# Optimization experiments

Measured on AMD Instinct MI355X. Metric: run time of the kernel, lower is better.

## Reference

```python
import jax, jax.numpy as jnp
import numpy as np

B, S, D = 2, 2048, 1024
H = 16
HEAD_DIM = 64          # matches head_dim init arg; D // H == 64
HALF_WINDOW = 32       # local_window_size // 2
SCALE = HEAD_DIM ** -0.5


def setup_inputs() -> dict:
    key = jax.random.key(0)
    ks = jax.random.split(key, 6)
    std = 1.0 / np.sqrt(D)
    return {
        "x": jax.random.normal(ks[0], (B, S, D), dtype=jnp.float32),
        "Wq": jax.random.normal(ks[1], (D, D), dtype=jnp.float32) * std,
        "Wk": jax.random.normal(ks[2], (D, D), dtype=jnp.float32) * std,
        "Wv": jax.random.normal(ks[3], (D, D), dtype=jnp.float32) * std,
        "Wo": jax.random.normal(ks[4], (D, D), dtype=jnp.float32) * std,
        "bo": jnp.zeros((D,), dtype=jnp.float32),
    }


def reference(x, Wq, Wk, Wv, Wo, bo):
    b, s, d = x.shape
    h, hd = H, d // H

    def split_heads(y):  # [b, s, d] -> [b, h, s, hd]
        return y.reshape(b, s, h, hd).transpose(0, 2, 1, 3)

    q = split_heads(x @ Wq) * SCALE
    k = split_heads(x @ Wk)
    v = split_heads(x @ Wv)

    # dense scores [b, h, s, s] (module materializes full O(S^2) matrix)
    scores = jnp.einsum("bhqd,bhkd->bhqk", q, k)

    # local window |i-j| <= HALF_WINDOW combined with causal j <= i
    i = jnp.arange(s)
    local = jnp.abs(i[:, None] - i[None, :]) <= HALF_WINDOW
    causal = i[None, :] <= i[:, None]
    mask = local & causal  # [s, s]
    scores = jnp.where(mask[None, None, :, :], scores, -jnp.inf)

    attn = jax.nn.softmax(scores, axis=-1)  # diagonal always valid -> no NaN
    out = jnp.einsum("bhqk,bhkd->bhqd", attn, v)
    out = out.transpose(0, 2, 1, 3).reshape(b, s, d)  # merge heads
    return out @ Wo + bo
```

## Files before the change

kernel.cpp:

```cpp
#include <hip/hip_runtime.h>
#include <hip/hip_bf16.h>

typedef __bf16 bf16_t;
typedef __bf16 bf16x8 __attribute__((ext_vector_type(8)));
typedef __bf16 bf16x4 __attribute__((ext_vector_type(4)));
typedef float  f32x4  __attribute__((ext_vector_type(4)));

#define B_   2
#define S_   2048
#define D_   1024
#define H_   16
#define HD_  64
#define HW   32
#define SCALE_ 0.125f

__device__ __forceinline__ void gl_lds16(const bf16_t* g, bf16_t* l) {
  __builtin_amdgcn_global_load_lds(
      (const __attribute__((address_space(1))) void*)g,
      (__attribute__((address_space(3))) void*)l, 16, 0, 0);
}

__global__ __launch_bounds__(256) void k_convert_x(const float* __restrict__ X,
                                                   bf16_t* __restrict__ Xb) {
  int i = blockIdx.x * 256 + threadIdx.x;
  const float4 a = ((const float4*)X)[i * 2];
  const float4 b = ((const float4*)X)[i * 2 + 1];
  bf16x8 r;
  r[0] = (bf16_t)a.x; r[1] = (bf16_t)a.y; r[2] = (bf16_t)a.z; r[3] = (bf16_t)a.w;
  r[4] = (bf16_t)b.x; r[5] = (bf16_t)b.y; r[6] = (bf16_t)b.z; r[7] = (bf16_t)b.w;
  ((bf16x8*)Xb)[i] = r;
}

__global__ __launch_bounds__(256) void k_convw(const float* __restrict__ W0,
                                               const float* __restrict__ W1,
                                               const float* __restrict__ W2,
                                               const float* __restrict__ W3,
                                               bf16_t* __restrict__ Wt) {
  __shared__ bf16_t t[64][72];
  int bid = blockIdx.x;
  int wsel = bid >> 8;
  const float* W = (wsel == 0) ? W0 : (wsel == 1) ? W1 : (wsel == 2) ? W2 : W3;
  bf16_t* dst = Wt + (size_t)wsel * D_ * D_;
  int tile = bid & 255;
  int k0 = (tile >> 4) * 64, n0 = (tile & 15) * 64;
  int tid = threadIdx.x;
  int r = tid >> 4, c4 = (tid & 15) * 4;
#pragma unroll
  for (int i = 0; i < 4; ++i) {
    int row = i * 16 + r;
    float4 v = *(const float4*)(W + (size_t)(k0 + row) * D_ + n0 + c4);
    t[row][c4 + 0] = (bf16_t)v.x;
    t[row][c4 + 1] = (bf16_t)v.y;
    t[row][c4 + 2] = (bf16_t)v.z;
    t[row][c4 + 3] = (bf16_t)v.w;
  }
  __syncthreads();
#pragma unroll
  for (int i = 0; i < 4; ++i) {
    int row = i * 16 + r;
    bf16x4 o;
    o[0] = t[c4 + 0][row];
    o[1] = t[c4 + 1][row];
    o[2] = t[c4 + 2][row];
    o[3] = t[c4 + 3][row];
    *(bf16x4*)(dst + (size_t)(n0 + row) * D_ + k0 + c4) = o;
  }
}

__global__ __launch_bounds__(256) void k_gemm_qkv(const bf16_t* __restrict__ X,
                                                  const bf16_t* __restrict__ Wt,
                                                  bf16_t* __restrict__ Q,
                                                  bf16_t* __restrict__ K,
                                                  bf16_t* __restrict__ V) {
  __shared__ bf16_t sA[128 * 32];
  __shared__ bf16_t sB[128 * 32];
  int bid = blockIdx.x;
  int mt = bid & 31, nt = bid >> 5;
  int wsel = nt >> 3;
  int n0 = (nt & 7) * 128, m0 = mt * 128;
  const bf16_t* Wp = Wt + (size_t)wsel * D_ * D_;
  int tid = threadIdx.x, lane = tid & 63, wave = tid >> 6;
  int wr = (wave >> 1) * 64, wc = (wave & 1) * 64;
  int r0 = wave * 32 + (lane >> 2);
  int ce = (lane & 3) * 8;
  const bf16_t* gA0 = X + (size_t)(m0 + r0) * D_ + ce;
  const bf16_t* gB0 = Wp + (size_t)(n0 + r0) * D_ + ce;
  bf16_t* lA0 = sA + wave * 1024;
  bf16_t* lB0 = sB + wave * 1024;
  f32x4 acc[4][4] = {};
  int kq = (lane >> 4) * 8, rl = lane & 15;
  for (int kt = 0; kt < D_; kt += 32) {
    __syncthreads();
    gl_lds16(gA0 + kt, lA0);
    gl_lds16(gA0 + kt + (size_t)16 * D_, lA0 + 512);
    gl_lds16(gB0 + kt, lB0);
    gl_lds16(gB0 + kt + (size_t)16 * D_, lB0 + 512);
    __syncthreads();
    bf16x8 af[4], bfr[4];
#pragma unroll
    for (int m = 0; m < 4; ++m)
      af[m] = *(const bf16x8*)&sA[(wr + m * 16 + rl) * 32 + kq];
#pragma unroll
    for (int n = 0; n < 4; ++n)
      bfr[n] = *(const bf16x8*)&sB[(wc + n * 16 + rl) * 32 + kq];
#pragma unroll
    for (int m = 0; m < 4; ++m)
#pragma unroll
      for (int n = 0; n < 4; ++n)
        acc[m][n] = __builtin_amdgcn_mfma_f32_16x16x32_bf16(af[m], bfr[n], acc[m][n], 0, 0, 0);
  }
  float qscale = (wsel == 0) ? SCALE_ : 1.0f;
#pragma unroll
  for (int m = 0; m < 4; ++m) {
#pragma unroll
    for (int n = 0; n < 4; ++n) {
#pragma unroll
      for (int r = 0; r < 4; ++r) {
        int gm = m0 + wr + m * 16 + (lane >> 4) * 4 + r;
        int gn = n0 + wc + n * 16 + rl;
        int b = gm >> 11, s = gm & 2047;
        int h = gn >> 6, hd = gn & 63;
        bf16_t val = (bf16_t)(acc[m][n][r] * qscale);
        if (wsel == 0)
          Q[(((size_t)(b * H_ + h)) * S_ + s) * HD_ + hd] = val;
        else if (wsel == 1)
          K[(((size_t)(b * H_ + h)) * S_ + s) * HD_ + hd] = val;
        else
          V[(((size_t)(b * H_ + h)) * HD_ + hd) * S_ + s] = val;
      }
    }
  }
}

__global__ __launch_bounds__(256) void k_gemm_out(const bf16_t* __restrict__ A,
                                                  const bf16_t* __restrict__ Wp,
                                                  const float* __restrict__ bo,
                                                  float* __restrict__ out) {
  __shared__ bf16_t sA[128 * 32];
  __shared__ bf16_t sB[128 * 32];
  int bid = blockIdx.x;
  int mt = bid & 31, nt = bid >> 5;
  int n0 = nt * 128, m0 = mt * 128;
  int tid = threadIdx.x, lane = tid & 63, wave = tid >> 6;
  int wr = (wave >> 1) * 64, wc = (wave & 1) * 64;
  int r0 = wave * 32 + (lane >> 2);
  int ce = (lane & 3) * 8;
  const bf16_t* gA0 = A + (size_t)(m0 + r0) * D_ + ce;
  const bf16_t* gB0 = Wp + (size_t)(n0 + r0) * D_ + ce;
  bf16_t* lA0 = sA + wave * 1024;
  bf16_t* lB0 = sB + wave * 1024;
  f32x4 acc[4][4] = {};
  int kq = (lane >> 4) * 8, rl = lane & 15;
  for (int kt = 0; kt < D_; kt += 32) {
    __syncthreads();
    gl_lds16(gA0 + kt, lA0);
    gl_lds16(gA0 + kt + (size_t)16 * D_, lA0 + 512);
    gl_lds16(gB0 + kt, lB0);
    gl_lds16(gB0 + kt + (size_t)16 * D_, lB0 + 512);
    __syncthreads();
    bf16x8 af[4], bfr[4];
#pragma unroll
    for (int m = 0; m < 4; ++m)
      af[m] = *(const bf16x8*)&sA[(wr + m * 16 + rl) * 32 + kq];
#pragma unroll
    for (int n = 0; n < 4; ++n)
      bfr[n] = *(const bf16x8*)&sB[(wc + n * 16 + rl) * 32 + kq];
#pragma unroll
    for (int m = 0; m < 4; ++m)
#pragma unroll
      for (int n = 0; n < 4; ++n)
        acc[m][n] = __builtin_amdgcn_mfma_f32_16x16x32_bf16(af[m], bfr[n], acc[m][n], 0, 0, 0);
  }
#pragma unroll
  for (int m = 0; m < 4; ++m) {
#pragma unroll
    for (int n = 0; n < 4; ++n) {
#pragma unroll
      for (int r = 0; r < 4; ++r) {
        int gm = m0 + wr + m * 16 + (lane >> 4) * 4 + r;
        int gn = n0 + wc + n * 16 + rl;
        out[(size_t)gm * D_ + gn] = acc[m][n][r] + bo[gn];
      }
    }
  }
}

#define QB 64
#define KW 112
#define KLP 72
#define VTP 120

__global__ __launch_bounds__(256) void k_attn(const bf16_t* __restrict__ Q,
                                              const bf16_t* __restrict__ K,
                                              const bf16_t* __restrict__ Vt,
                                              bf16_t* __restrict__ O) {
  __shared__ bf16_t sK[KW][KLP];
  __shared__ bf16_t sV[HD_][VTP];
  __shared__ bf16_t sQ[QB][KLP];
  __shared__ bf16_t sP[4][16][KLP];
  int bid = blockIdx.x;
  int qb = bid & 31, bh = bid >> 5;
  int q0 = qb * QB;
  const bf16_t* Kp = K + (size_t)bh * S_ * HD_;
  const bf16_t* Vp = Vt + (size_t)bh * HD_ * S_;
  const bf16_t* Qp = Q + (size_t)bh * S_ * HD_;
  int tid = threadIdx.x;
  int wk0b = q0 - HW;
  for (int idx = tid; idx < KW * 8; idx += 256) {
    int row = idx >> 3, c8 = (idx & 7) * 8;
    int kg = wk0b + row;
    kg = kg < 0 ? 0 : (kg > S_ - 1 ? S_ - 1 : kg);
    *(bf16x8*)&sK[row][c8] = *(const bf16x8*)(Kp + (size_t)kg * HD_ + c8);
  }
  for (int idx = tid; idx < HD_ * 14; idx += 256) {
    int row = idx / 14, c8 = (idx % 14) * 8;
    int ks = wk0b + c8;
    ks = ks < 0 ? 0 : (ks > S_ - 8 ? S_ - 8 : ks);
    *(bf16x8*)&sV[row][c8] = *(const bf16x8*)(Vp + (size_t)row * S_ + ks);
  }
  for (int idx = tid; idx < QB * 8; idx += 256) {
    int row = idx >> 3, c8 = (idx & 7) * 8;
    *(bf16x8*)&sQ[row][c8] = *(const bf16x8*)(Qp + (size_t)(q0 + row) * HD_ + c8);
  }
  __syncthreads();
  int lane = tid & 63, wave = tid >> 6;
  int rl = lane & 15, hi = lane >> 4;
  int wko = wave * 16;
  f32x4 accs[4] = {};
#pragma unroll
  for (int ds = 0; ds < 2; ++ds) {
    bf16x8 qf = *(const bf16x8*)&sQ[wave * 16 + rl][ds * 32 + hi * 8];
#pragma unroll
    for (int kb = 0; kb < 4; ++kb) {
      bf16x8 kf = *(const bf16x8*)&sK[wko + kb * 16 + rl][ds * 32 + hi * 8];
      accs[kb] = __builtin_amdgcn_mfma_f32_16x16x32_bf16(kf, qf, accs[kb], 0, 0, 0);
    }
  }
  float p[4][4];
  float mx = -1e30f;
#pragma unroll
  for (int kb = 0; kb < 4; ++kb) {
#pragma unroll
    for (int r = 0; r < 4; ++r) {
      int kl = kb * 16 + hi * 4 + r;
      bool valid = (kl >= rl) && (kl <= rl + HW) && (wk0b + wko + kl >= 0);
      float s = valid ? accs[kb][r] : -1e30f;
      p[kb][r] = s;
      mx = fmaxf(mx, s);
    }
  }
  mx = fmaxf(mx, __shfl_xor(mx, 16));
  mx = fmaxf(mx, __shfl_xor(mx, 32));
  float sum = 0.f;
#pragma unroll
  for (int kb = 0; kb < 4; ++kb)
#pragma unroll
    for (int r = 0; r < 4; ++r) {
      p[kb][r] = __expf(p[kb][r] - mx);
      sum += p[kb][r];
    }
  sum += __shfl_xor(sum, 16);
  sum += __shfl_xor(sum, 32);
  float inv = 1.f / sum;
#pragma unroll
  for (int kb = 0; kb < 4; ++kb) {
    bf16x4 pv;
#pragma unroll
    for (int r = 0; r < 4; ++r) pv[r] = (bf16_t)(p[kb][r] * inv);
    *(bf16x4*)&sP[wave][rl][kb * 16 + hi * 4] = pv;
  }
  f32x4 acco[4] = {};
#pragma unroll
  for (int ks = 0; ks < 2; ++ks) {
    bf16x8 aP = *(const bf16x8*)&sP[wave][rl][ks * 32 + hi * 8];
#pragma unroll
    for (int n = 0; n < 4; ++n) {
      bf16x8 bV = *(const bf16x8*)&sV[n * 16 + rl][wko + ks * 32 + hi * 8];
      acco[n] = __builtin_amdgcn_mfma_f32_16x16x32_bf16(aP, bV, acco[n], 0, 0, 0);
    }
  }
  int b = bh >> 4, h = bh & 15;
#pragma unroll
  for (int n = 0; n < 4; ++n) {
#pragma unroll
    for (int r = 0; r < 4; ++r) {
      int qgl = q0 + wave * 16 + hi * 4 + r;
      int d = n * 16 + rl;
      O[((size_t)(b * S_ + qgl)) * D_ + h * HD_ + d] = (bf16_t)acco[n][r];
    }
  }
}

extern "C" void kernel_launch(void* const* d_in, const int* in_sizes, int n_in,
                              void* d_out, int out_size, void* d_ws, size_t ws_size,
                              hipStream_t stream) {
  const float* x  = (const float*)d_in[0];
  const float* Wq = (const float*)d_in[1];
  const float* Wk = (const float*)d_in[2];
  const float* Wv = (const float*)d_in[3];
  const float* Wo = (const float*)d_in[4];
  const float* bo = (const float*)d_in[5];
  float* out = (float*)d_out;
  char* ws = (char*)d_ws;
  bf16_t* xb = (bf16_t*)(ws);
  bf16_t* wt = (bf16_t*)(ws + (size_t)(8 << 20));
  bf16_t* qb = (bf16_t*)(ws + (size_t)(16 << 20));
  bf16_t* kb = (bf16_t*)(ws + (size_t)(24 << 20));
  bf16_t* vb = (bf16_t*)(ws + (size_t)(32 << 20));
  bf16_t* ob = (bf16_t*)(ws + (size_t)(40 << 20));

  hipLaunchKernelGGL(k_convert_x, dim3(2048), dim3(256), 0, stream, x, xb);
  hipLaunchKernelGGL(k_convw, dim3(1024), dim3(256), 0, stream, Wq, Wk, Wv, Wo, wt);
  hipLaunchKernelGGL(k_gemm_qkv, dim3(768), dim3(256), 0, stream, xb, wt, qb, kb, vb);
  hipLaunchKernelGGL(k_attn, dim3(1024), dim3(256), 0, stream, qb, kb, vb, ob);
  hipLaunchKernelGGL(k_gemm_out, dim3(256), dim3(256), 0, stream,
                     ob, wt + (size_t)3 * D_ * D_, bo, out);
}
```

Measured before the change: 88.24 us.

## Double-buffer GEMM LDS loads, vectorize QKV stores via LDS, merge conversion kernels

Both GEMM kernels now double-buffer their LDS tiles, so the next K-slice loads while MFMAs run on the current one, and each iteration needs one barrier instead of two. The QKV epilogue stages results through an LDS bounce buffer so Q/K and the transposed V are written as 16-byte vector stores rather than scattered 2-byte stores. The x and weight conversion kernels are merged into one launch. The cost is double the LDS per block, which may reduce occupancy, plus extra barriers in the epilogue.

```diff
diff --git a/kernel.cpp b/kernel.cpp
--- a/kernel.cpp
+++ b/kernel.cpp
@@ -13,6 +13,8 @@
 #define HD_  64
 #define HW   32
 #define SCALE_ 0.125f
+#define NT_  32
+#define BPAD 136
 
 __device__ __forceinline__ void gl_lds16(const bf16_t* g, bf16_t* l) {
   __builtin_amdgcn_global_load_lds(
@@ -20,30 +22,32 @@
       (__attribute__((address_space(3))) void*)l, 16, 0, 0);
 }
 
-__global__ __launch_bounds__(256) void k_convert_x(const float* __restrict__ X,
-                                                   bf16_t* __restrict__ Xb) {
-  int i = blockIdx.x * 256 + threadIdx.x;
-  const float4 a = ((const float4*)X)[i * 2];
-  const float4 b = ((const float4*)X)[i * 2 + 1];
-  bf16x8 r;
-  r[0] = (bf16_t)a.x; r[1] = (bf16_t)a.y; r[2] = (bf16_t)a.z; r[3] = (bf16_t)a.w;
-  r[4] = (bf16_t)b.x; r[5] = (bf16_t)b.y; r[6] = (bf16_t)b.z; r[7] = (bf16_t)b.w;
-  ((bf16x8*)Xb)[i] = r;
-}
-
-__global__ __launch_bounds__(256) void k_convw(const float* __restrict__ W0,
-                                               const float* __restrict__ W1,
-                                               const float* __restrict__ W2,
-                                               const float* __restrict__ W3,
-                                               bf16_t* __restrict__ Wt) {
+__global__ __launch_bounds__(256) void k_conv(const float* __restrict__ X,
+                                              const float* __restrict__ W0,
+                                              const float* __restrict__ W1,
+                                              const float* __restrict__ W2,
+                                              const float* __restrict__ W3,
+                                              bf16_t* __restrict__ Xb,
+                                              bf16_t* __restrict__ Wt) {
   __shared__ bf16_t t[64][72];
   int bid = blockIdx.x;
-  int wsel = bid >> 8;
+  int tid = threadIdx.x;
+  if (bid < 2048) {
+    int i = bid * 256 + tid;
+    const float4 a = ((const float4*)X)[i * 2];
+    const float4 b = ((const float4*)X)[i * 2 + 1];
+    bf16x8 r;
+    r[0] = (bf16_t)a.x; r[1] = (bf16_t)a.y; r[2] = (bf16_t)a.z; r[3] = (bf16_t)a.w;
+    r[4] = (bf16_t)b.x; r[5] = (bf16_t)b.y; r[6] = (bf16_t)b.z; r[7] = (bf16_t)b.w;
+    ((bf16x8*)Xb)[i] = r;
+    return;
+  }
+  int wb = bid - 2048;
+  int wsel = wb >> 8;
   const float* W = (wsel == 0) ? W0 : (wsel == 1) ? W1 : (wsel == 2) ? W2 : W3;
   bf16_t* dst = Wt + (size_t)wsel * D_ * D_;
-  int tile = bid & 255;
+  int tile = wb & 255;
   int k0 = (tile >> 4) * 64, n0 = (tile & 15) * 64;
-  int tid = threadIdx.x;
   int r = tid >> 4, c4 = (tid & 15) * 4;
 #pragma unroll
   for (int i = 0; i < 4; ++i) {
@@ -72,8 +76,7 @@
                                                   bf16_t* __restrict__ Q,
                                                   bf16_t* __restrict__ K,
                                                   bf16_t* __restrict__ V) {
-  __shared__ bf16_t sA[128 * 32];
-  __shared__ bf16_t sB[128 * 32];
+  __shared__ bf16_t smem[4][128 * 32];
   int bid = blockIdx.x;
   int mt = bid & 31, nt = bid >> 5;
   int wsel = nt >> 3;
@@ -85,48 +88,89 @@
   int ce = (lane & 3) * 8;
   const bf16_t* gA0 = X + (size_t)(m0 + r0) * D_ + ce;
   const bf16_t* gB0 = Wp + (size_t)(n0 + r0) * D_ + ce;
-  bf16_t* lA0 = sA + wave * 1024;
-  bf16_t* lB0 = sB + wave * 1024;
+  int lofs = wave * 1024;
   f32x4 acc[4][4] = {};
-  int kq = (lane >> 4) * 8, rl = lane & 15;
-  for (int kt = 0; kt < D_; kt += 32) {
-    __syncthreads();
-    gl_lds16(gA0 + kt, lA0);
-    gl_lds16(gA0 + kt + (size_t)16 * D_, lA0 + 512);
-    gl_lds16(gB0 + kt, lB0);
-    gl_lds16(gB0 + kt + (size_t)16 * D_, lB0 + 512);
-    __syncthreads();
+  int kq = (lane >> 4) * 8, rl = lane & 15, hi = lane >> 4;
+  gl_lds16(gA0, &smem[0][lofs]);
+  gl_lds16(gA0 + (size_t)16 * D_, &smem[0][lofs + 512]);
+  gl_lds16(gB0, &smem[2][lofs]);
+  gl_lds16(gB0 + (size_t)16 * D_, &smem[2][lofs + 512]);
+  __syncthreads();
+  int cur = 0;
+  for (int t = 0; t < NT_; ++t) {
+    if (t + 1 < NT_) {
+      int kt = (t + 1) * 32, nb = cur ^ 1;
+      gl_lds16(gA0 + kt, &smem[nb][lofs]);
+      gl_lds16(gA0 + kt + (size_t)16 * D_, &smem[nb][lofs + 512]);
+      gl_lds16(gB0 + kt, &smem[2 + nb][lofs]);
+      gl_lds16(gB0 + kt + (size_t)16 * D_, &smem[2 + nb][lofs + 512]);
+    }
     bf16x8 af[4], bfr[4];
 #pragma unroll
     for (int m = 0; m < 4; ++m)
-      af[m] = *(const bf16x8*)&sA[(wr + m * 16 + rl) * 32 + kq];
+      af[m] = *(const bf16x8*)&smem[cur][(wr + m * 16 + rl) * 32 + kq];
 #pragma unroll
     for (int n = 0; n < 4; ++n)
-      bfr[n] = *(const bf16x8*)&sB[(wc + n * 16 + rl) * 32 + kq];
+      bfr[n] = *(const bf16x8*)&smem[2 + cur][(wc + n * 16 + rl) * 32 + kq];
 #pragma unroll
     for (int m = 0; m < 4; ++m)
 #pragma unroll
       for (int n = 0; n < 4; ++n)
         acc[m][n] = __builtin_amdgcn_mfma_f32_16x16x32_bf16(af[m], bfr[n], acc[m][n], 0, 0, 0);
-  }
-  float qscale = (wsel == 0) ? SCALE_ : 1.0f;
-#pragma unroll
-  for (int m = 0; m < 4; ++m) {
-#pragma unroll
-    for (int n = 0; n < 4; ++n) {
-#pragma unroll
-      for (int r = 0; r < 4; ++r) {
-        int gm = m0 + wr + m * 16 + (lane >> 4) * 4 + r;
-        int gn = n0 + wc + n * 16 + rl;
-        int b = gm >> 11, s = gm & 2047;
-        int h = gn >> 6, hd = gn & 63;
-        bf16_t val = (bf16_t)(acc[m][n][r] * qscale);
-        if (wsel == 0)
-          Q[(((size_t)(b * H_ + h)) * S_ + s) * HD_ + hd] = val;
-        else if (wsel == 1)
-          K[(((size_t)(b * H_ + h)) * S_ + s) * HD_ + hd] = val;
-        else
-          V[(((size_t)(b * H_ + h)) * HD_ + hd) * S_ + s] = val;
+    __syncthreads();
+    cur ^= 1;
+  }
+  bf16_t* bounce = &smem[0][0];
+  if (wsel < 2) {
+    bf16_t* Dst = wsel ? K : Q;
+    float qs = wsel ? 1.0f : SCALE_;
+#pragma unroll
+    for (int hh = 0; hh < 2; ++hh) {
+      if (hh) __syncthreads();
+      if ((wr >> 6) == hh) {
+#pragma unroll
+        for (int m = 0; m < 4; ++m)
+#pragma unroll
+          for (int n = 0; n < 4; ++n)
+#pragma unroll
+            for (int r = 0; r < 4; ++r)
+              bounce[(m * 16 + hi * 4 + r) * BPAD + wc + n * 16 + rl] =
+                  (bf16_t)(acc[m][n][r] * qs);
+      }
+      __syncthreads();
+#pragma unroll
+      for (int ps = 0; ps < 4; ++ps) {
+        int idx = ps * 256 + tid;
+        int row = idx >> 4, c8 = (idx & 15) * 8;
+        bf16x8 v = *(const bf16x8*)&bounce[row * BPAD + c8];
+        int gm = m0 + hh * 64 + row, gn = n0 + c8;
+        int b = gm >> 11, s = gm & 2047, h = gn >> 6, hd = gn & 63;
+        *(bf16x8*)&Dst[(((size_t)(b * H_ + h)) * S_ + s) * HD_ + hd] = v;
+      }
+    }
+  } else {
+#pragma unroll
+    for (int hh = 0; hh < 2; ++hh) {
+      if (hh) __syncthreads();
+      if ((wc >> 6) == hh) {
+#pragma unroll
+        for (int m = 0; m < 4; ++m)
+#pragma unroll
+          for (int n = 0; n < 4; ++n)
+#pragma unroll
+            for (int r = 0; r < 4; ++r)
+              bounce[(n * 16 + rl) * BPAD + wr + m * 16 + hi * 4 + r] =
+                  (bf16_t)acc[m][n][r];
+      }
+      __syncthreads();
+#pragma unroll
+      for (int ps = 0; ps < 4; ++ps) {
+        int idx = ps * 256 + tid;
+        int row = idx >> 4, c8 = (idx & 15) * 8;
+        bf16x8 v = *(const bf16x8*)&bounce[row * BPAD + c8];
+        int gn = n0 + hh * 64 + row, gmS = m0 + c8;
+        int b = gmS >> 11, s0 = gmS & 2047, h = gn >> 6, hd = gn & 63;
+        *(bf16x8*)&V[(((size_t)(b * H_ + h)) * HD_ + hd) * S_ + s0] = v;
       }
     }
   }
@@ -136,8 +180,7 @@
                                                   const bf16_t* __restrict__ Wp,
                                                   const float* __restrict__ bo,
                                                   float* __restrict__ out) {
-  __shared__ bf16_t sA[128 * 32];
-  __shared__ bf16_t sB[128 * 32];
+  __shared__ bf16_t smem[4][128 * 32];
   int bid = blockIdx.x;
   int mt = bid & 31, nt = bid >> 5;
   int n0 = nt * 128, m0 = mt * 128;
@@ -147,29 +190,37 @@
   int ce = (lane & 3) * 8;
   const bf16_t* gA0 = A + (size_t)(m0 + r0) * D_ + ce;
   const bf16_t* gB0 = Wp + (size_t)(n0 + r0) * D_ + ce;
-  bf16_t* lA0 = sA + wave * 1024;
-  bf16_t* lB0 = sB + wave * 1024;
+  int lofs = wave * 1024;
   f32x4 acc[4][4] = {};
   int kq = (lane >> 4) * 8, rl = lane & 15;
-  for (int kt = 0; kt < D_; kt += 32) {
-    __syncthreads();
-    gl_lds16(gA0 + kt, lA0);
-    gl_lds16(gA0 + kt + (size_t)16 * D_, lA0 + 512);
-    gl_lds16(gB0 + kt, lB0);
-    gl_lds16(gB0 + kt + (size_t)16 * D_, lB0 + 512);
-    __syncthreads();
+  gl_lds16(gA0, &smem[0][lofs]);
+  gl_lds16(gA0 + (size_t)16 * D_, &smem[0][lofs + 512]);
+  gl_lds16(gB0, &smem[2][lofs]);
+  gl_lds16(gB0 + (size_t)16 * D_, &smem[2][lofs + 512]);
+  __syncthreads();
+  int cur = 0;
+  for (int t = 0; t < NT_; ++t) {
+    if (t + 1 < NT_) {
+      int kt = (t + 1) * 32, nb = cur ^ 1;
+      gl_lds16(gA0 + kt, &smem[nb][lofs]);
+      gl_lds16(gA0 + kt + (size_t)16 * D_, &smem[nb][lofs + 512]);
+      gl_lds16(gB0 + kt, &smem[2 + nb][lofs]);
+      gl_lds16(gB0 + kt + (size_t)16 * D_, &smem[2 + nb][lofs + 512]);
+    }
     bf16x8 af[4], bfr[4];
 #pragma unroll
     for (int m = 0; m < 4; ++m)
-      af[m] = *(const bf16x8*)&sA[(wr + m * 16 + rl) * 32 + kq];
+      af[m] = *(const bf16x8*)&smem[cur][(wr + m * 16 + rl) * 32 + kq];
 #pragma unroll
     for (int n = 0; n < 4; ++n)
-      bfr[n] = *(const bf16x8*)&sB[(wc + n * 16 + rl) * 32 + kq];
+      bfr[n] = *(const bf16x8*)&smem[2 + cur][(wc + n * 16 + rl) * 32 + kq];
 #pragma unroll
     for (int m = 0; m < 4; ++m)
 #pragma unroll
       for (int n = 0; n < 4; ++n)
         acc[m][n] = __builtin_amdgcn_mfma_f32_16x16x32_bf16(af[m], bfr[n], acc[m][n], 0, 0, 0);
+    __syncthreads();
+    cur ^= 1;
   }
 #pragma unroll
   for (int m = 0; m < 4; ++m) {
@@ -309,8 +360,8 @@
   bf16_t* vb = (bf16_t*)(ws + (size_t)(32 << 20));
   bf16_t* ob = (bf16_t*)(ws + (size_t)(40 << 20));
 
-  hipLaunchKernelGGL(k_convert_x, dim3(2048), dim3(256), 0, stream, x, xb);
-  hipLaunchKernelGGL(k_convw, dim3(1024), dim3(256), 0, stream, Wq, Wk, Wv, Wo, wt);
+  hipLaunchKernelGGL(k_conv, dim3(3072), dim3(256), 0, stream,
+                     x, Wq, Wk, Wv, Wo, xb, wt);
   hipLaunchKernelGGL(k_gemm_qkv, dim3(768), dim3(256), 0, stream, xb, wt, qb, kb, vb);
   hipLaunchKernelGGL(k_attn, dim3(1024), dim3(256), 0, stream, qb, kb, vb, ob);
   hipLaunchKernelGGL(k_gemm_out, dim3(256), dim3(256), 0, stream,
```

After: 89.03 us. No clear change (+0.9%).
